# Kernel optimization log

Measured on AMD Instinct MI355X. Metric: run time of the kernel, lower is better.

Reference implementation:

```python
import jax, jax.numpy as jnp
import numpy as np

# Routing structure from the torch module
GT0 = [[0,1,0,0,1,0],[0,1,0,0,0,1],[0,0,1,0,1,0],[0,0,1,0,0,1],[0,0,0,1,1,0],[0,0,0,1,0,1]]
NCLS = 6
K = 1  # top-k

def _expert_pairs():
    # For class i, expert index m = 1+(j-1)*5+(k-1) maps to atom1[j-1] -> atom2[k-1].
    pairs = []
    for i in range(NCLS):
        p = [(j - 1, k - 1) for j in range(1, 6) for k in range(1, 6)
             if j != k and GT0[i][j] == 1 and GT0[i][k] == 1]
        pairs.append(p)
    return pairs

PAIRS = _expert_pairs()  # each class has exactly 2 (atom1, atom2) pairs

B, P, D, H = 64, 256, 768, 3072

def setup_inputs() -> dict:
    key = jax.random.key(0)
    ks = jax.random.split(key, 8)
    s = 0.02
    x = jax.random.normal(ks[0], (B, NCLS + P, D), dtype=jnp.float32)
    mids = jax.random.randint(ks[1], (B,), 0, 6)
    moe0_W1 = jax.random.normal(ks[2], (D, H), dtype=jnp.float32) * s
    moe0_b1 = jnp.zeros((H,), jnp.float32)
    moe0_W2 = jax.random.normal(ks[3], (H, D), dtype=jnp.float32) * s
    moe0_b2 = jnp.zeros((D,), jnp.float32)
    A1_W = jax.random.normal(ks[4], (5, D, H), dtype=jnp.float32) * s  # atom1 linears
    A1_b = jnp.zeros((5, H), jnp.float32)
    A2_W = jax.random.normal(ks[5], (5, H, D), dtype=jnp.float32) * s  # atom2 linears
    A2_b = jnp.zeros((5, D), jnp.float32)
    G_W = jax.random.normal(ks[6], (NCLS, D, 2), dtype=jnp.float32) * s  # per-class gates (2 experts each, no bias)
    return {"x": x, "moe0_W1": moe0_W1, "moe0_b1": moe0_b1, "moe0_W2": moe0_W2,
            "moe0_b2": moe0_b2, "A1_W": A1_W, "A1_b": A1_b, "A2_W": A2_W,
            "A2_b": A2_b, "G_W": G_W, "mids": mids}

def _gelu(t):
    return jax.nn.gelu(t, approximate=False)  # torch nn.GELU default = erf

def reference(x, moe0_W1, moe0_b1, moe0_W2, moe0_b2, A1_W, A1_b, A2_W, A2_b, G_W, mids):
    cls_tokens = x[:, :NCLS]          # [B, 6, D]
    patch_tokens = x[:, NCLS:]        # [B, P, D]
    patch_out = _gelu(patch_tokens @ moe0_W1 + moe0_b1) @ moe0_W2 + moe0_b2  # [B, P, D]
    cls_outs = []
    for i in range(NCLS):
        tok = cls_tokens[:, i]        # [B, D]
        eouts = [ _gelu(tok @ A1_W[a] + A1_b[a]) @ A2_W[c] + A2_b[c] for (a, c) in PAIRS[i] ]
        out = jnp.stack(eouts, axis=-1)                 # [B, D, E=2]
        gate = jax.nn.softmax(tok @ G_W[i], axis=-1)    # [B, E]
        # top-k masking (k=1 < E=2): keep gates strictly above the (k+1)-th largest
        thr = jnp.sort(gate, axis=-1)[..., -(K + 1)]    # [B]
        mask = (gate > thr[..., None]).astype(gate.dtype)
        g = gate * mask
        g = g / jnp.clip(jnp.sum(g, axis=-1, keepdims=True), 1e-6)
        cls_outs.append(jnp.sum(out * g[:, None, :], axis=-1))  # [B, D]
    cls_out = jnp.stack(cls_outs, axis=1)               # [B, 6, D]
    return jnp.concatenate([cls_out, patch_out], axis=1)  # [B, 6+P, D]
```

## Files before the change

### kernel.cpp

```cpp
#include <hip/hip_runtime.h>
#include <hip/hip_bf16.h>

#define DD 768
#define HH 3072
#define BB 64
#define TT 262

typedef __bf16 bf16x8 __attribute__((ext_vector_type(8)));
typedef float f32x4 __attribute__((ext_vector_type(4)));
typedef unsigned short u16;
typedef unsigned int u32;

__device__ __constant__ int A_FIRST[12]  = {0,3, 0,4, 1,3, 1,4, 2,3, 2,4};
__device__ __constant__ int A_SECOND[12] = {3,0, 4,0, 3,1, 4,1, 3,2, 4,2};

__device__ __forceinline__ float gelu_f(float x) {
  float n2t = x * fmaf(x * x, -0.0713548163f, -1.5957691216f);
  return x * __builtin_amdgcn_rcpf(1.0f + __expf(n2t));
}

__device__ __forceinline__ u16 f2bf(float x) {
  u32 u = __builtin_bit_cast(u32, x);
  return (u16)((u + 0x7fffu + ((u >> 16) & 1u)) >> 16);
}

__device__ __forceinline__ void load_lds16(const void* g, void* l) {
  __builtin_amdgcn_global_load_lds(
      (const __attribute__((address_space(1))) void*)g,
      (__attribute__((address_space(3))) void*)l,
      16, 0, 0);
}

__global__ __launch_bounds__(256)
void preproc(const float* __restrict__ x,
             const float* __restrict__ W1, const float* __restrict__ A1W,
             const float* __restrict__ W2, const float* __restrict__ A2W,
             const float* __restrict__ GW,
             __hip_bfloat16* __restrict__ xb,
             __hip_bfloat16* __restrict__ W1t, __hip_bfloat16* __restrict__ A1t,
             __hip_bfloat16* __restrict__ W2t, __hip_bfloat16* __restrict__ A2t,
             int* __restrict__ sel) {
  __shared__ __hip_bfloat16 tile[32][33];
  const int bx = blockIdx.x;
  const int tid = threadIdx.x;
  if (bx < 12576) {
    int i = bx * 256 + tid;
    float4 v = ((const float4*)x)[i];
    union { u16 s[4]; uint2 d; } pk;
    pk.s[0] = f2bf(v.x); pk.s[1] = f2bf(v.y); pk.s[2] = f2bf(v.z); pk.s[3] = f2bf(v.w);
    *(uint2*)((u16*)xb + (size_t)i * 4) = pk.d;
  } else if (bx < 40224) {
    int R, C;
    const float* ip;
    __hip_bfloat16* op;
    int t;
    if (bx < 26400) {
      t = bx - 12576; R = DD; C = HH;
      int z = t / 2304; t %= 2304;
      ip = z ? (A1W + (size_t)(z - 1) * DD * HH) : W1;
      op = z ? (A1t + (size_t)(z - 1) * DD * HH) : W1t;
    } else {
      t = bx - 26400; R = HH; C = DD;
      int z = t / 2304; t %= 2304;
      ip = z ? (A2W + (size_t)(z - 1) * DD * HH) : W2;
      op = z ? (A2t + (size_t)(z - 1) * DD * HH) : W2t;
    }
    int ctiles = C >> 5;
    int c0 = (t % ctiles) * 32, r0 = (t / ctiles) * 32;
    int tx = tid & 31, ty = tid >> 5;
#pragma unroll
    for (int s = 0; s < 4; ++s) {
      int rr = ty * 4 + s;
      tile[rr][tx] = __float2bfloat16(ip[(size_t)(r0 + rr) * C + c0 + tx]);
    }
    __syncthreads();
#pragma unroll
    for (int s = 0; s < 4; ++s) {
      int cc = ty * 4 + s;
      op[(size_t)(c0 + cc) * R + r0 + tx] = tile[tx][cc];
    }
  } else {
    int unit = (bx - 40224) * 4 + (tid >> 6);
    int lane = tid & 63;
    int b = unit & 63, i = unit >> 6;
    const float* tok = x + (size_t)(b * TT + i) * DD;
    const float* g = GW + (size_t)i * DD * 2;
    float p0 = 0.f, p1 = 0.f;
    for (int k = lane; k < DD; k += 64) {
      float tv = tok[k];
      p0 += tv * g[k * 2 + 0];
      p1 += tv * g[k * 2 + 1];
    }
#pragma unroll
    for (int o = 32; o; o >>= 1) { p0 += __shfl_xor(p0, o); p1 += __shfl_xor(p1, o); }
    if (lane == 0) sel[i * 64 + b] = (p0 > p1) ? 0 : ((p1 > p0) ? 1 : 2);
  }
}

template <int BM, int BN, int MODE>
__device__ __forceinline__
void gemm_body(char* __restrict__ smem, int bx,
               const __hip_bfloat16* __restrict__ A,
               const __hip_bfloat16* __restrict__ Bw,
               const float* __restrict__ bias,
               void* __restrict__ Out,
               const int* __restrict__ sel) {
  constexpr int KDIM = (MODE == 0 || MODE == 2) ? DD : HH;
  constexpr int KITERS = KDIM / 64;
  constexpr int WAVES_M = (BM == 128) ? 2 : 1;
  constexpr int WAVES_N = 4 / WAVES_M;
  constexpr int MT = BM / (16 * WAVES_M);
  constexpr int NT = BN / (16 * WAVES_N);
  constexpr int CHA = BM / 32;
  constexpr int CHB = BN / 32;

  char* As = smem;
  char* Bs = smem + BM * 128;

  const int tid = threadIdx.x;
  const int lane = tid & 63;
  const int wave = tid >> 6;
  const int q = lane >> 4;
  const int r = lane & 15;
  const int wave_m = wave / WAVES_N;
  const int wave_n = wave % WAVES_N;

  int m0 = 0, n0, combo = 0, cls_i = 0;
  const __hip_bfloat16* Bp = Bw;
  const float* biasp = bias;
  if constexpr (MODE == 0) {
    int chunk = bx / 192, local = bx % 192;
    int nb = local / 16, mloc = local % 16;
    m0 = (chunk * 16 + mloc) * BM;
    n0 = nb * BN;
  } else if constexpr (MODE == 1) {
    int chunk = bx / 96, local = bx % 96;
    int nb = local / 16, mloc = local % 16;
    m0 = (chunk * 16 + mloc) * BM;
    n0 = nb * BN;
  } else if constexpr (MODE == 2) {
    n0 = (bx % 24) * BN;
    combo = bx / 24;
    cls_i = combo >> 1;
    int e = A_FIRST[combo];
    Bp = Bw + (size_t)e * DD * HH;
    biasp = bias + e * HH;
  } else {
    n0 = (bx % 6) * BN;
    combo = bx / 6;
    cls_i = combo >> 1;
    int e = A_SECOND[combo];
    Bp = Bw + (size_t)e * DD * HH;
    biasp = bias + e * DD;
  }

  const int trow = tid >> 3;
  const int sw = ((tid & 7) ^ (trow & 7)) << 4;
  size_t a_row_off;
  if constexpr (MODE == 0) {
    int m = m0 + trow;
    a_row_off = (size_t)((m >> 8) * TT + 6 + (m & 255)) * DD * 2;
  } else if constexpr (MODE == 1) {
    a_row_off = (size_t)(m0 + trow) * HH * 2;
  } else if constexpr (MODE == 2) {
    a_row_off = (size_t)(trow * TT + cls_i) * DD * 2;
  } else {
    a_row_off = (size_t)(combo * 64 + trow) * HH * 2;
  }
  const char* gA0 = (const char*)A + a_row_off + sw;
  const char* gB0 = (const char*)Bp + (size_t)(n0 + trow) * KDIM * 2 + sw;
  constexpr size_t ASTR = (size_t)32 * ((MODE == 0) ? DD : (MODE == 2) ? TT * DD : HH) * 2;
  constexpr size_t BSTR = (size_t)32 * KDIM * 2;
  const int wave_base = (tid & ~63) * 16;

  f32x4 acc[MT][NT];
#pragma unroll
  for (int i_ = 0; i_ < MT; ++i_)
#pragma unroll
    for (int j_ = 0; j_ < NT; ++j_) acc[i_][j_] = (f32x4){0.f, 0.f, 0.f, 0.f};

  const char* a_rd = As + (wave_m * (MT * 16) + r) * 128;
  const char* b_rd = Bs + (wave_n * (NT * 16) + r) * 128;
  const int sa = ((q ^ (r & 7)) << 4);

  for (int kt = 0; kt < KITERS; ++kt) {
#pragma unroll
    for (int u = 0; u < CHA; ++u) load_lds16(gA0 + u * ASTR, As + u * 4096 + wave_base);
#pragma unroll
    for (int u = 0; u < CHB; ++u) load_lds16(gB0 + u * BSTR, Bs + u * 4096 + wave_base);
    gA0 += 128;
    gB0 += 128;
    __syncthreads();
#pragma unroll
    for (int t = 0; t < 2; ++t) {
      const int so = sa ^ (t << 6);
      bf16x8 af[MT], bf[NT];
#pragma unroll
      for (int i_ = 0; i_ < MT; ++i_) af[i_] = *(const bf16x8*)(a_rd + i_ * 2048 + so);
#pragma unroll
      for (int j_ = 0; j_ < NT; ++j_) bf[j_] = *(const bf16x8*)(b_rd + j_ * 2048 + so);
#pragma unroll
      for (int i_ = 0; i_ < MT; ++i_)
#pragma unroll
        for (int j_ = 0; j_ < NT; ++j_)
          acc[i_][j_] = __builtin_amdgcn_mfma_f32_16x16x32_bf16(bf[j_], af[i_], acc[i_][j_], 0, 0, 0);
    }
    __syncthreads();
  }

#pragma unroll
  for (int i_ = 0; i_ < MT; ++i_) {
    int m_g = m0 + wave_m * (MT * 16) + i_ * 16 + r;
#pragma unroll
    for (int j_ = 0; j_ < NT; ++j_) {
      int nb = n0 + wave_n * (NT * 16) + j_ * 16 + q * 4;
      f32x4 v = acc[i_][j_];
      f32x4 bb = *(const f32x4*)(biasp + nb);
      v += bb;
      if constexpr (MODE == 0) {
        union { u16 s[4]; uint2 d; } pk;
#pragma unroll
        for (int rg = 0; rg < 4; ++rg) pk.s[rg] = f2bf(gelu_f(v[rg]));
        *(uint2*)((u16*)Out + (size_t)m_g * HH + nb) = pk.d;
      } else if constexpr (MODE == 1) {
        int b = m_g >> 8, p = m_g & 255;
        *(f32x4*)((float*)Out + (size_t)(b * TT + 6 + p) * DD + nb) = v;
      } else if constexpr (MODE == 2) {
        union { u16 s[4]; uint2 d; } pk;
#pragma unroll
        for (int rg = 0; rg < 4; ++rg) pk.s[rg] = f2bf(gelu_f(v[rg]));
        *(uint2*)((u16*)Out + (size_t)(combo * 64 + m_g) * HH + nb) = pk.d;
      } else {
        int s = sel[cls_i * 64 + m_g];
        int j = combo & 1;
        float* dst = (float*)Out + (size_t)(m_g * TT + cls_i) * DD + nb;
        if (s == j) {
          *(f32x4*)dst = v;
        } else if (j == 0 && s == 2) {
          *(f32x4*)dst = (f32x4){0.f, 0.f, 0.f, 0.f};
        }
      }
    }
  }
}

__global__ __launch_bounds__(256, 2)
void mega1(const __hip_bfloat16* __restrict__ xb, const __hip_bfloat16* __restrict__ W1t,
           const float* __restrict__ b1, __hip_bfloat16* __restrict__ hid,
           const __hip_bfloat16* __restrict__ A1t, const float* __restrict__ A1b,
           __hip_bfloat16* __restrict__ hcls) {
  __shared__ __align__(16) char smem[(128 + 256) * 128];
  int bx = blockIdx.x;
  if (bx < 1536) gemm_body<128, 256, 0>(smem, bx, xb, W1t, b1, hid, nullptr);
  else           gemm_body<64, 128, 2>(smem, bx - 1536, xb, A1t, A1b, hcls, nullptr);
}

__global__ __launch_bounds__(256, 2)
void mega2(const __hip_bfloat16* __restrict__ hid, const __hip_bfloat16* __restrict__ W2t,
           const float* __restrict__ b2, float* __restrict__ out,
           const __hip_bfloat16* __restrict__ hcls, const __hip_bfloat16* __restrict__ A2t,
           const float* __restrict__ A2b, const int* __restrict__ sel) {
  __shared__ __align__(16) char smem[(128 + 128) * 128];
  int bx = blockIdx.x;
  if (bx < 768) gemm_body<128, 128, 1>(smem, bx, hid, W2t, b2, out, nullptr);
  else          gemm_body<64, 128, 3>(smem, bx - 768, hcls, A2t, A2b, out, sel);
}

extern "C" void kernel_launch(void* const* d_in, const int* in_sizes, int n_in,
                              void* d_out, int out_size, void* d_ws, size_t ws_size,
                              hipStream_t stream) {
  const float* x   = (const float*)d_in[0];
  const float* W1  = (const float*)d_in[1];
  const float* b1  = (const float*)d_in[2];
  const float* W2  = (const float*)d_in[3];
  const float* b2  = (const float*)d_in[4];
  const float* A1W = (const float*)d_in[5];
  const float* A1b = (const float*)d_in[6];
  const float* A2W = (const float*)d_in[7];
  const float* A2b = (const float*)d_in[8];
  const float* GW  = (const float*)d_in[9];
  float* out = (float*)d_out;

  char* ws = (char*)d_ws;
  __hip_bfloat16* xb   = (__hip_bfloat16*)(ws + 0);
  __hip_bfloat16* W1t  = (__hip_bfloat16*)(ws + 25755648);
  __hip_bfloat16* W2t  = (__hip_bfloat16*)(ws + 30474240);
  __hip_bfloat16* A1t  = (__hip_bfloat16*)(ws + 35192832);
  __hip_bfloat16* A2t  = (__hip_bfloat16*)(ws + 58785792);
  __hip_bfloat16* hcls = (__hip_bfloat16*)(ws + 82378752);
  int* sel             = (int*)(ws + 87097344);
  __hip_bfloat16* hid  = (__hip_bfloat16*)(ws + 87099136);

  preproc<<<40320, 256, 0, stream>>>(x, W1, A1W, W2, A2W, GW, xb, W1t, A1t, W2t, A2t, sel);
  mega1<<<1824, 256, 0, stream>>>(xb, W1t, b1, hid, A1t, A1b, hcls);
  mega2<<<840, 256, 0, stream>>>(hid, W2t, b2, out, hcls, A2t, A2b, sel);
}
```

Baseline: 392.0 us.

## Split preprocessing into wider-tile weight transpose and vectorized cast/gate kernels

The monolithic preproc kernel is split in two. A weight-transpose kernel now uses 64x64 tiles with float4 global loads and 16-byte bf16 stores through a padded LDS tile. A separate cast/gate kernel converts x to bf16 eight elements per thread and computes the gate selection. The aim is to cut the cost of the memory-bound weight conversion and transpose, which previously used 32x32 tiles with scalar 2-byte stores. The trade-off is one extra kernel launch and more LDS traffic per block.

```diff
diff --git a/kernel.cpp b/kernel.cpp
--- a/kernel.cpp
+++ b/kernel.cpp
@@ -5,6 +5,7 @@
 #define HH 3072
 #define BB 64
 #define TT 262
+#define DH (DD * HH)
 
 typedef __bf16 bf16x8 __attribute__((ext_vector_type(8)));
 typedef float f32x4 __attribute__((ext_vector_type(4)));
@@ -32,55 +33,66 @@
 }
 
 __global__ __launch_bounds__(256)
-void preproc(const float* __restrict__ x,
-             const float* __restrict__ W1, const float* __restrict__ A1W,
-             const float* __restrict__ W2, const float* __restrict__ A2W,
-             const float* __restrict__ GW,
-             __hip_bfloat16* __restrict__ xb,
-             __hip_bfloat16* __restrict__ W1t, __hip_bfloat16* __restrict__ A1t,
-             __hip_bfloat16* __restrict__ W2t, __hip_bfloat16* __restrict__ A2t,
-             int* __restrict__ sel) {
-  __shared__ __hip_bfloat16 tile[32][33];
-  const int bx = blockIdx.x;
-  const int tid = threadIdx.x;
-  if (bx < 12576) {
-    int i = bx * 256 + tid;
-    float4 v = ((const float4*)x)[i];
-    union { u16 s[4]; uint2 d; } pk;
-    pk.s[0] = f2bf(v.x); pk.s[1] = f2bf(v.y); pk.s[2] = f2bf(v.z); pk.s[3] = f2bf(v.w);
-    *(uint2*)((u16*)xb + (size_t)i * 4) = pk.d;
-  } else if (bx < 40224) {
-    int R, C;
-    const float* ip;
-    __hip_bfloat16* op;
-    int t;
-    if (bx < 26400) {
-      t = bx - 12576; R = DD; C = HH;
-      int z = t / 2304; t %= 2304;
-      ip = z ? (A1W + (size_t)(z - 1) * DD * HH) : W1;
-      op = z ? (A1t + (size_t)(z - 1) * DD * HH) : W1t;
-    } else {
-      t = bx - 26400; R = HH; C = DD;
-      int z = t / 2304; t %= 2304;
-      ip = z ? (A2W + (size_t)(z - 1) * DD * HH) : W2;
-      op = z ? (A2t + (size_t)(z - 1) * DD * HH) : W2t;
-    }
-    int ctiles = C >> 5;
-    int c0 = (t % ctiles) * 32, r0 = (t / ctiles) * 32;
-    int tx = tid & 31, ty = tid >> 5;
-#pragma unroll
-    for (int s = 0; s < 4; ++s) {
-      int rr = ty * 4 + s;
-      tile[rr][tx] = __float2bfloat16(ip[(size_t)(r0 + rr) * C + c0 + tx]);
-    }
-    __syncthreads();
-#pragma unroll
-    for (int s = 0; s < 4; ++s) {
-      int cc = ty * 4 + s;
-      op[(size_t)(c0 + cc) * R + r0 + tx] = tile[tx][cc];
-    }
+void wtrans(const float* __restrict__ W1, const float* __restrict__ A1W,
+            const float* __restrict__ W2, const float* __restrict__ A2W,
+            u16* __restrict__ W1t, u16* __restrict__ A1t,
+            u16* __restrict__ W2t, u16* __restrict__ A2t) {
+  __shared__ u16 tileT[64 * 68];
+  const int bx = blockIdx.x, tid = threadIdx.x;
+  const int mat = bx / 576, t = bx % 576;
+  const float* ip;
+  u16* op;
+  int R, C;
+  if (mat < 6) {
+    R = DD; C = HH;
+    ip = mat ? A1W + (size_t)(mat - 1) * DH : W1;
+    op = mat ? A1t + (size_t)(mat - 1) * DH : W1t;
   } else {
-    int unit = (bx - 40224) * 4 + (tid >> 6);
+    int z = mat - 6;
+    R = HH; C = DD;
+    ip = z ? A2W + (size_t)(z - 1) * DH : W2;
+    op = z ? A2t + (size_t)(z - 1) * DH : W2t;
+  }
+  const int ct = C >> 6;
+  const int r0 = (t / ct) << 6, c0 = (t % ct) << 6;
+  const int rr = tid >> 4;
+  const int cg = (tid & 15) << 2;
+#pragma unroll
+  for (int it = 0; it < 4; ++it) {
+    int row = rr + (it << 4);
+    float4 v = *(const float4*)(ip + (size_t)(r0 + row) * C + c0 + cg);
+    tileT[(cg + 0) * 68 + row] = f2bf(v.x);
+    tileT[(cg + 1) * 68 + row] = f2bf(v.y);
+    tileT[(cg + 2) * 68 + row] = f2bf(v.z);
+    tileT[(cg + 3) * 68 + row] = f2bf(v.w);
+  }
+  __syncthreads();
+#pragma unroll
+  for (int it = 0; it < 2; ++it) {
+    int u = (it << 8) + tid;
+    int oc = u >> 3, seg = (u & 7) << 3;
+    const u16* src = tileT + oc * 68 + seg;
+    uint2 lo = *(const uint2*)(src);
+    uint2 hi = *(const uint2*)(src + 4);
+    uint4 val = make_uint4(lo.x, lo.y, hi.x, hi.y);
+    *(uint4*)(op + (size_t)(c0 + oc) * R + r0 + seg) = val;
+  }
+}
+
+__global__ __launch_bounds__(256)
+void castgate(const float* __restrict__ x, const float* __restrict__ GW,
+              u16* __restrict__ xb, int* __restrict__ sel) {
+  const int bx = blockIdx.x, tid = threadIdx.x;
+  if (bx < 6288) {
+    size_t i = ((size_t)bx * 256 + tid) * 2;
+    float4 v0 = ((const float4*)x)[i];
+    float4 v1 = ((const float4*)x)[i + 1];
+    union { u16 s[8]; uint4 d; } pk;
+    pk.s[0] = f2bf(v0.x); pk.s[1] = f2bf(v0.y); pk.s[2] = f2bf(v0.z); pk.s[3] = f2bf(v0.w);
+    pk.s[4] = f2bf(v1.x); pk.s[5] = f2bf(v1.y); pk.s[6] = f2bf(v1.z); pk.s[7] = f2bf(v1.w);
+    *(uint4*)(xb + i * 4) = pk.d;
+  } else {
+    int unit = (bx - 6288) * 4 + (tid >> 6);
     int lane = tid & 63;
     int b = unit & 63, i = unit >> 6;
     const float* tok = x + (size_t)(b * TT + i) * DD;
@@ -143,14 +155,14 @@
     combo = bx / 24;
     cls_i = combo >> 1;
     int e = A_FIRST[combo];
-    Bp = Bw + (size_t)e * DD * HH;
+    Bp = Bw + (size_t)e * DH;
     biasp = bias + e * HH;
   } else {
     n0 = (bx % 6) * BN;
     combo = bx / 6;
     cls_i = combo >> 1;
     int e = A_SECOND[combo];
-    Bp = Bw + (size_t)e * DD * HH;
+    Bp = Bw + (size_t)e * DH;
     biasp = bias + e * DD;
   }
 
@@ -291,7 +303,9 @@
   int* sel             = (int*)(ws + 87097344);
   __hip_bfloat16* hid  = (__hip_bfloat16*)(ws + 87099136);
 
-  preproc<<<40320, 256, 0, stream>>>(x, W1, A1W, W2, A2W, GW, xb, W1t, A1t, W2t, A2t, sel);
+  wtrans<<<6912, 256, 0, stream>>>(W1, A1W, W2, A2W,
+                                   (u16*)W1t, (u16*)A1t, (u16*)W2t, (u16*)A2t);
+  castgate<<<6384, 256, 0, stream>>>(x, GW, (u16*)xb, sel);
   mega1<<<1824, 256, 0, stream>>>(xb, W1t, b1, hid, A1t, A1b, hcls);
   mega2<<<840, 256, 0, stream>>>(hid, W2t, b2, out, hcls, A2t, A2b, sel);
 }
```

Measured after the change: 404.4 us. 3.2% more time.
